# Kernel tuning notes

Measured on AMD Instinct MI355X. Metric: run time of the kernel, lower is better.

The kernel has to match this reference:

```python
import jax, jax.numpy as jnp
import numpy as np

N = 100000   # nodes
E = 3200000  # edges (avg degree 32)
G = 1024     # graphs in batch
H = 16       # hidden_dim


def setup_inputs() -> dict:
    key = jax.random.key(0)
    ks = jax.random.split(key, 12)
    p = lambda k, s: jax.random.normal(k, s, dtype=jnp.float32) * 0.1
    return {
        "types": jax.random.randint(ks[0], (N,), 0, 3),
        "pos": jax.random.randint(ks[1], (N,), 0, 3),
        "edge_index": jax.random.randint(ks[2], (2, E), 0, N),
        "batch": jnp.sort(jax.random.randint(ks[3], (N,), 0, G)),
        "W1": p(ks[4], (3, H)), "b1": jnp.zeros((H,), jnp.float32),
        "W2": p(ks[5], (3, H)), "b2": jnp.zeros((H,), jnp.float32),
        "Wg0": p(ks[6], (2 * H, H)), "bg0": jnp.zeros((H,), jnp.float32),
        "Wg1": p(ks[7], (H, H)), "bg1": jnp.zeros((H,), jnp.float32),
        "Wg2": p(ks[8], (H, H)), "bg2": jnp.zeros((H,), jnp.float32),
        "Wo": p(ks[9], (H, 1)), "bo": jnp.zeros((1,), jnp.float32),
    }


def reference(types, pos, edge_index, batch, W1, b1, W2, b2,
              Wg0, bg0, Wg1, bg1, Wg2, bg2, Wo, bo):
    # one-hot encode + linear embed
    xt = jax.nn.one_hot(types, 3, dtype=jnp.float32) @ W1 + b1   # [N, H]
    xp = jax.nn.one_hot(pos, 3, dtype=jnp.float32) @ W2 + b2     # [N, H]
    z = jnp.concatenate([xt, xp], axis=-1)                        # [N, 2H]

    src, dst = edge_index[0], edge_index[1]
    # GCN symmetric normalization with self-loops (gcn_norm)
    deg = jax.ops.segment_sum(jnp.ones((E,), jnp.float32), dst, num_segments=N) + 1.0
    dis = jax.lax.rsqrt(deg)                                      # D^{-1/2}
    edge_coef = (dis[src] * dis[dst])[:, None]                    # [E, 1]
    self_coef = (dis * dis)[:, None]                              # [N, 1]

    def gcn_conv(x, W, b):
        h = x @ W                                                 # [N, H]
        agg = jax.ops.segment_sum(h[src] * edge_coef, dst, num_segments=N)
        return agg + h * self_coef + b

    z = jax.nn.relu(gcn_conv(z, Wg0, bg0))  # dropout=0.2 is train-only; eval mode
    z = jax.nn.relu(gcn_conv(z, Wg1, bg1))
    z = gcn_conv(z, Wg2, bg2)               # no act after last layer

    # global_mean_pool over graph ids
    cnt = jax.ops.segment_sum(jnp.ones((N,), jnp.float32), batch, num_segments=G)
    pooled = jax.ops.segment_sum(z, batch, num_segments=G) / jnp.maximum(cnt, 1.0)[:, None]
    return pooled @ Wo + bo                                       # [G, 1]
```

## Files before the change

### kernel.cpp

```cpp
#include <hip/hip_runtime.h>
#include <hip/hip_fp16.h>

#define NN 100000
#define NE 3200000
#define NG 1024
#define NP 100352
#define NBUCK 391
#define NBLK 256
#define CHUNK ((NE + NBLK - 1) / NBLK)
#define WINCAP 12288
#define BATCH 8

static __device__ inline void acc8_u4(float* acc, uint4 u) {
    const __half2* ph = reinterpret_cast<const __half2*>(&u);
#pragma unroll
    for (int k = 0; k < 4; k++) {
        float2 f = __half22float2(ph[k]);
        acc[2 * k + 0] += f.x;
        acc[2 * k + 1] += f.y;
    }
}
static __device__ inline uint4 pack8(const float* v) {
    uint4 u;
    __half2 h0 = __floats2half2_rn(v[0], v[1]);
    __half2 h1 = __floats2half2_rn(v[2], v[3]);
    __half2 h2 = __floats2half2_rn(v[4], v[5]);
    __half2 h3 = __floats2half2_rn(v[6], v[7]);
    u.x = *reinterpret_cast<unsigned int*>(&h0);
    u.y = *reinterpret_cast<unsigned int*>(&h1);
    u.z = *reinterpret_cast<unsigned int*>(&h2);
    u.w = *reinterpret_cast<unsigned int*>(&h3);
    return u;
}

__global__ void hist_buckets(const int* __restrict__ dst, int* __restrict__ bcnt) {
    __shared__ int sm[NBUCK];
    int tid = threadIdx.x;
    for (int i = tid; i < NBUCK; i += 256) sm[i] = 0;
    __syncthreads();
    int s = blockIdx.x * CHUNK, e = min(NE, s + CHUNK);
    for (int i = s + tid; i < e; i += 256)
        atomicAdd(&sm[__builtin_nontemporal_load(&dst[i]) >> 8], 1);
    __syncthreads();
    for (int i = tid; i < NBUCK; i += 256)
        if (sm[i]) atomicAdd(&bcnt[i], sm[i]);
}

__global__ void scan_buckets(const int* __restrict__ bcnt, int* __restrict__ bbase) {
    __shared__ int tmp[512];
    int tid = threadIdx.x;
    int v = (tid < NBUCK) ? bcnt[tid] : 0;
    tmp[tid] = v;
    __syncthreads();
    for (int off = 1; off < 512; off <<= 1) {
        int t = (tid >= off) ? tmp[tid - off] : 0;
        __syncthreads();
        tmp[tid] += t;
        __syncthreads();
    }
    if (tid < NBUCK) bbase[tid] = tmp[tid] - v;
}

__global__ void partition(const int* __restrict__ src, const int* __restrict__ dst,
                          const int* __restrict__ bbase, int* __restrict__ bfill,
                          int* __restrict__ part) {
    __shared__ int smh[NBUCK];
    __shared__ int smc[NBUCK];
    int tid = threadIdx.x;
    for (int i = tid; i < NBUCK; i += 256) smh[i] = 0;
    __syncthreads();
    int s = blockIdx.x * CHUNK, e = min(NE, s + CHUNK);
    for (int i = s + tid; i < e; i += 256)
        atomicAdd(&smh[__builtin_nontemporal_load(&dst[i]) >> 8], 1);
    __syncthreads();
    for (int i = tid; i < NBUCK; i += 256) {
        int c = smh[i];
        smc[i] = c ? (bbase[i] + atomicAdd(&bfill[i], c)) : 0;
    }
    __syncthreads();
    for (int i = s + tid; i < e; i += 256) {
        int d = __builtin_nontemporal_load(&dst[i]);
        int sv = __builtin_nontemporal_load(&src[i]);
        int b = d >> 8;
        int p = atomicAdd(&smc[b], 1);
        part[p] = sv | ((d & 255) << 17);
    }
}

__global__ void build_csr(const int* __restrict__ part, const int* __restrict__ bbase,
                          const int* __restrict__ bcnt, int* __restrict__ cnt,
                          int* __restrict__ offs, float* __restrict__ dis,
                          int* __restrict__ srcs) {
    __shared__ int sm_cnt[256];
    __shared__ int sm_off[256];
    __shared__ int sm_cur[256];
    __shared__ int sm_win[WINCAP];
    int b = blockIdx.x, tid = threadIdx.x;
    int base = bbase[b], m = bcnt[b];
    sm_cnt[tid] = 0;
    __syncthreads();
    for (int i = tid; i < m; i += 256)
        atomicAdd(&sm_cnt[__builtin_nontemporal_load(&part[base + i]) >> 17], 1);
    __syncthreads();
    int v = sm_cnt[tid];
    sm_off[tid] = v;
    __syncthreads();
    for (int off = 1; off < 256; off <<= 1) {
        int t = (tid >= off) ? sm_off[tid - off] : 0;
        __syncthreads();
        sm_off[tid] += t;
        __syncthreads();
    }
    int excl = sm_off[tid] - v;
    int n = b * 256 + tid;
    if (n < NN) {
        cnt[n] = v;
        offs[n] = base + excl;
        dis[n] = rsqrtf((float)v + 1.0f);
    }
    sm_cur[tid] = excl;
    __syncthreads();
    if (m <= WINCAP) {
        for (int i = tid; i < m; i += 256) {
            int p = __builtin_nontemporal_load(&part[base + i]);
            int l = atomicAdd(&sm_cur[p >> 17], 1);
            sm_win[l] = p & 0x1FFFF;
        }
        __syncthreads();
        for (int i = tid; i < m; i += 256) srcs[base + i] = sm_win[i];
    } else {
        for (int i = tid; i < m; i += 256) {
            int p = __builtin_nontemporal_load(&part[base + i]);
            int l = atomicAdd(&sm_cur[p >> 17], 1);
            srcs[base + l] = p & 0x1FFFF;
        }
    }
}

__global__ void embed_tf0(const int* __restrict__ types, const int* __restrict__ pos,
                          const float* __restrict__ W1, const float* __restrict__ b1,
                          const float* __restrict__ W2, const float* __restrict__ b2,
                          const float* __restrict__ Wg0, const float* __restrict__ dis,
                          uint4* __restrict__ hs) {
    __shared__ float sW[32 * 16];
    int tid = threadIdx.x;
    sW[tid] = Wg0[tid];
    sW[tid + 256] = Wg0[tid + 256];
    __syncthreads();
    int n = blockIdx.x * 256 + tid;
    if (n >= NN) return;
    int ty = types[n], pp = pos[n];
    float z[32];
#pragma unroll
    for (int j = 0; j < 16; j++) z[j] = W1[ty * 16 + j] + b1[j];
#pragma unroll
    for (int j = 0; j < 16; j++) z[16 + j] = W2[pp * 16 + j] + b2[j];
    float dn = dis[n];
    float hv[16];
#pragma unroll
    for (int j = 0; j < 16; j++) {
        float a = 0.0f;
#pragma unroll
        for (int k = 0; k < 32; k++) a += z[k] * sW[k * 16 + j];
        hv[j] = a * dn;
    }
    hs[(size_t)n * 2 + 0] = pack8(hv);
    hs[(size_t)n * 2 + 1] = pack8(hv + 8);
}

template <int RELU, int FUSE_POOL>
__global__ __launch_bounds__(256, 4)
void agg_tf(const uint4* __restrict__ hs, const int* __restrict__ srcs,
            const int* __restrict__ offs, const int* __restrict__ cnt,
            const float* __restrict__ dis, const float* __restrict__ bias,
            const float* __restrict__ Wn, uint4* __restrict__ hs_out,
            const int* __restrict__ batch,
            float* __restrict__ pool, int* __restrict__ gcnt) {
    __shared__ float sW[256];
    int tid = threadIdx.x;
    if (!FUSE_POOL) {
        sW[tid] = Wn[tid];
        __syncthreads();
    }
    int gid = blockIdx.x * 256 + tid;
    int n = gid >> 2;
    int q = gid & 1;
    int c = (gid >> 1) & 1;
    if (n >= NN) return;
    int beg = offs[n], deg = cnt[n];
    float dn = dis[n];
    int half = deg >> 1;
    int i0 = c ? half : 0;
    int iend = c ? deg : half;
    float acc[8] = {0.f, 0.f, 0.f, 0.f, 0.f, 0.f, 0.f, 0.f};
    for (int i = i0; i < iend; i += BATCH) {
        uint4 g[BATCH];
#pragma unroll
        for (int j = 0; j < BATCH; j++) {
            int idx = i + j;
            int s = __builtin_nontemporal_load(&srcs[beg + idx]);
            s = (idx < iend) ? s : NN;
            g[j] = hs[(size_t)s * 2 + q];
        }
#pragma unroll
        for (int j = 0; j < BATCH; j++) acc8_u4(acc, g[j]);
    }
#pragma unroll
    for (int k = 0; k < 8; k++) acc[k] += __shfl_xor(acc[k], 2);
    if (c != 0) return;
    uint4 self = hs[(size_t)n * 2 + q];
    acc8_u4(acc, self);
#pragma unroll
    for (int k = 0; k < 8; k++) {
        acc[k] = fmaf(acc[k], dn, bias[q * 8 + k]);
        if (RELU) acc[k] = fmaxf(acc[k], 0.f);
    }
    if (FUSE_POOL) {
        float s = 0.f;
#pragma unroll
        for (int k = 0; k < 8; k++) s += acc[k] * Wn[q * 8 + k];
        s += __shfl_xor(s, 1);
        if (q == 0) {
            int g = batch[n];
            atomicAdd(&pool[g], s);
            atomicAdd(&gcnt[g], 1);
        }
    } else {
        float oth[8];
#pragma unroll
        for (int k = 0; k < 8; k++) oth[k] = __shfl_xor(acc[k], 1);
        float zlo[8], zhi[8];
#pragma unroll
        for (int k = 0; k < 8; k++) {
            zlo[k] = (q == 0) ? acc[k] : oth[k];
            zhi[k] = (q == 0) ? oth[k] : acc[k];
        }
        float hv[8] = {0.f, 0.f, 0.f, 0.f, 0.f, 0.f, 0.f, 0.f};
#pragma unroll
        for (int k = 0; k < 8; k++) {
            const float* wl = &sW[k * 16 + q * 8];
            const float* wh = &sW[(k + 8) * 16 + q * 8];
#pragma unroll
            for (int j = 0; j < 8; j++) {
                hv[j] += zlo[k] * wl[j];
                hv[j] += zhi[k] * wh[j];
            }
        }
#pragma unroll
        for (int j = 0; j < 8; j++) hv[j] *= dn;
        hs_out[(size_t)n * 2 + q] = pack8(hv);
    }
}

__global__ void finalize(const float* __restrict__ pool, const int* __restrict__ gcnt,
                         const float* __restrict__ bo, float* __restrict__ out) {
    int g = blockIdx.x * 256 + threadIdx.x;
    if (g < NG) {
        float c = fmaxf((float)gcnt[g], 1.0f);
        out[g] = pool[g] / c + bo[0];
    }
}

extern "C" void kernel_launch(void* const* d_in, const int* in_sizes, int n_in,
                              void* d_out, int out_size, void* d_ws, size_t ws_size,
                              hipStream_t stream) {
    const int*   types = (const int*)d_in[0];
    const int*   pos   = (const int*)d_in[1];
    const int*   ei    = (const int*)d_in[2];
    const int*   batch = (const int*)d_in[3];
    const float* W1  = (const float*)d_in[4];
    const float* b1  = (const float*)d_in[5];
    const float* W2  = (const float*)d_in[6];
    const float* b2  = (const float*)d_in[7];
    const float* Wg0 = (const float*)d_in[8];
    const float* bg0 = (const float*)d_in[9];
    const float* Wg1 = (const float*)d_in[10];
    const float* bg1 = (const float*)d_in[11];
    const float* Wg2 = (const float*)d_in[12];
    const float* bg2 = (const float*)d_in[13];
    const float* Wo  = (const float*)d_in[14];
    const float* bo  = (const float*)d_in[15];
    float* out = (float*)d_out;

    const int* esrc = ei;
    const int* edst = ei + NE;

    int*   bcnt  = (int*)d_ws;
    int*   bfill = bcnt + 512;
    float* pool  = (float*)(bfill + 512);
    int*   gcnt  = (int*)(pool + NG);
    int*   bbase = gcnt + NG;
    int*   cnt   = bbase + 512;
    int*   offs  = cnt + NP;
    float* dis   = (float*)(offs + NP);
    int*   srcs  = (int*)(dis + NP);
    int*   part  = srcs + NE;
    uint4* hsA   = (uint4*)part;
    uint4* hsB   = (uint4*)(part + NE / 2);
    (void)ws_size; (void)n_in; (void)in_sizes; (void)out_size;

    hipMemsetAsync(d_ws, 0, (size_t)(1024 + 2 * NG) * sizeof(int), stream);

    const int NB256 = (NN + 255) / 256;
    const int QB4 = (NN * 4 + 255) / 256;

    hist_buckets<<<NBLK, 256, 0, stream>>>(edst, bcnt);
    scan_buckets<<<1, 512, 0, stream>>>(bcnt, bbase);
    partition<<<NBLK, 256, 0, stream>>>(esrc, edst, bbase, bfill, part);
    build_csr<<<NBUCK, 256, 0, stream>>>(part, bbase, bcnt, cnt, offs, dis, srcs);

    hipMemsetAsync((char*)hsA + (size_t)NN * 32, 0, (size_t)(NP - NN) * 32, stream);
    hipMemsetAsync((char*)hsB + (size_t)NN * 32, 0, (size_t)(NP - NN) * 32, stream);

    embed_tf0<<<NB256, 256, 0, stream>>>(types, pos, W1, b1, W2, b2, Wg0, dis, hsA);
    agg_tf<1, 0><<<QB4, 256, 0, stream>>>(hsA, srcs, offs, cnt, dis, bg0, Wg1, hsB,
                                          batch, pool, gcnt);
    agg_tf<1, 0><<<QB4, 256, 0, stream>>>(hsB, srcs, offs, cnt, dis, bg1, Wg2, hsA,
                                          batch, pool, gcnt);
    agg_tf<0, 1><<<QB4, 256, 0, stream>>>(hsA, srcs, offs, cnt, dis, bg2, Wo, hsB ,
                                          batch, pool, gcnt);

    finalize<<<(NG + 255) / 256, 256, 0, stream>>>(pool, gcnt, bo, out);
}
```

Measured before the change: 342.7 us.

## Split neighbor list four ways per node, gathering full 32-byte rows

The aggregation kernel now gives each of four lanes per node a quarter of the edge list, and each lane loads the full 32-byte fp16 row of every neighbor instead of one half-row. Before, two lanes split the edges and each loaded one 16-byte half, so every source index was read twice. Now each index is read once and the 16-wide sums are combined across the four lanes with shuffles. The row gathers become nontemporal loads while the index loads become normal ones, and launch bounds drop to 3 blocks per CU to fit 16 accumulators and twice as many in-flight loads.

Measured after the change: 533.3 us. 55.6% more time.

```diff
diff --git a/kernel.cpp b/kernel.cpp
--- a/kernel.cpp
+++ b/kernel.cpp
@@ -11,25 +11,28 @@
 #define WINCAP 12288
 #define BATCH 8
 
-static __device__ inline void acc8_u4(float* acc, uint4 u) {
-    const __half2* ph = reinterpret_cast<const __half2*>(&u);
+typedef unsigned int u32x4 __attribute__((ext_vector_type(4)));
+
+static __device__ inline void acc8_v4(float* acc, u32x4 u) {
 #pragma unroll
     for (int k = 0; k < 4; k++) {
-        float2 f = __half22float2(ph[k]);
+        unsigned int w = u[k];
+        __half2 h = *reinterpret_cast<__half2*>(&w);
+        float2 f = __half22float2(h);
         acc[2 * k + 0] += f.x;
         acc[2 * k + 1] += f.y;
     }
 }
-static __device__ inline uint4 pack8(const float* v) {
-    uint4 u;
+static __device__ inline u32x4 pack8(const float* v) {
+    u32x4 u;
     __half2 h0 = __floats2half2_rn(v[0], v[1]);
     __half2 h1 = __floats2half2_rn(v[2], v[3]);
     __half2 h2 = __floats2half2_rn(v[4], v[5]);
     __half2 h3 = __floats2half2_rn(v[6], v[7]);
-    u.x = *reinterpret_cast<unsigned int*>(&h0);
-    u.y = *reinterpret_cast<unsigned int*>(&h1);
-    u.z = *reinterpret_cast<unsigned int*>(&h2);
-    u.w = *reinterpret_cast<unsigned int*>(&h3);
+    u[0] = *reinterpret_cast<unsigned int*>(&h0);
+    u[1] = *reinterpret_cast<unsigned int*>(&h1);
+    u[2] = *reinterpret_cast<unsigned int*>(&h2);
+    u[3] = *reinterpret_cast<unsigned int*>(&h3);
     return u;
 }
 
@@ -141,7 +144,7 @@
                           const float* __restrict__ W1, const float* __restrict__ b1,
                           const float* __restrict__ W2, const float* __restrict__ b2,
                           const float* __restrict__ Wg0, const float* __restrict__ dis,
-                          uint4* __restrict__ hs) {
+                          u32x4* __restrict__ hs) {
     __shared__ float sW[32 * 16];
     int tid = threadIdx.x;
     sW[tid] = Wg0[tid];
@@ -169,11 +172,11 @@
 }
 
 template <int RELU, int FUSE_POOL>
-__global__ __launch_bounds__(256, 4)
-void agg_tf(const uint4* __restrict__ hs, const int* __restrict__ srcs,
+__global__ __launch_bounds__(256, 3)
+void agg_tf(const u32x4* __restrict__ hs, const int* __restrict__ srcs,
             const int* __restrict__ offs, const int* __restrict__ cnt,
             const float* __restrict__ dis, const float* __restrict__ bias,
-            const float* __restrict__ Wn, uint4* __restrict__ hs_out,
+            const float* __restrict__ Wn, u32x4* __restrict__ hs_out,
             const int* __restrict__ batch,
             float* __restrict__ pool, int* __restrict__ gcnt) {
     __shared__ float sW[256];
@@ -184,71 +187,69 @@
     }
     int gid = blockIdx.x * 256 + tid;
     int n = gid >> 2;
-    int q = gid & 1;
-    int c = (gid >> 1) & 1;
+    int c = gid & 3;
     if (n >= NN) return;
     int beg = offs[n], deg = cnt[n];
     float dn = dis[n];
-    int half = deg >> 1;
-    int i0 = c ? half : 0;
-    int iend = c ? deg : half;
-    float acc[8] = {0.f, 0.f, 0.f, 0.f, 0.f, 0.f, 0.f, 0.f};
+    int i0 = (deg * c) >> 2;
+    int iend = (deg * (c + 1)) >> 2;
+    float acc[16];
+#pragma unroll
+    for (int k = 0; k < 16; k++) acc[k] = 0.f;
     for (int i = i0; i < iend; i += BATCH) {
-        uint4 g[BATCH];
+        u32x4 g0[BATCH], g1[BATCH];
 #pragma unroll
         for (int j = 0; j < BATCH; j++) {
             int idx = i + j;
-            int s = __builtin_nontemporal_load(&srcs[beg + idx]);
+            int s = srcs[beg + idx];
             s = (idx < iend) ? s : NN;
-            g[j] = hs[(size_t)s * 2 + q];
-        }
-#pragma unroll
-        for (int j = 0; j < BATCH; j++) acc8_u4(acc, g[j]);
-    }
-#pragma unroll
-    for (int k = 0; k < 8; k++) acc[k] += __shfl_xor(acc[k], 2);
-    if (c != 0) return;
-    uint4 self = hs[(size_t)n * 2 + q];
-    acc8_u4(acc, self);
-#pragma unroll
-    for (int k = 0; k < 8; k++) {
-        acc[k] = fmaf(acc[k], dn, bias[q * 8 + k]);
+            const u32x4* row = &hs[(size_t)s * 2];
+            g0[j] = __builtin_nontemporal_load(row);
+            g1[j] = __builtin_nontemporal_load(row + 1);
+        }
+#pragma unroll
+        for (int j = 0; j < BATCH; j++) {
+            acc8_v4(acc, g0[j]);
+            acc8_v4(acc + 8, g1[j]);
+        }
+    }
+#pragma unroll
+    for (int k = 0; k < 16; k++) acc[k] += __shfl_xor(acc[k], 1);
+#pragma unroll
+    for (int k = 0; k < 16; k++) acc[k] += __shfl_xor(acc[k], 2);
+    u32x4 s0 = hs[(size_t)n * 2 + 0];
+    u32x4 s1 = hs[(size_t)n * 2 + 1];
+    acc8_v4(acc, s0);
+    acc8_v4(acc + 8, s1);
+#pragma unroll
+    for (int k = 0; k < 16; k++) {
+        acc[k] = fmaf(acc[k], dn, bias[k]);
         if (RELU) acc[k] = fmaxf(acc[k], 0.f);
     }
     if (FUSE_POOL) {
-        float s = 0.f;
-#pragma unroll
-        for (int k = 0; k < 8; k++) s += acc[k] * Wn[q * 8 + k];
-        s += __shfl_xor(s, 1);
-        if (q == 0) {
+        if (c == 0) {
+            float s = 0.f;
+#pragma unroll
+            for (int k = 0; k < 16; k++) s += acc[k] * Wn[k];
             int g = batch[n];
             atomicAdd(&pool[g], s);
             atomicAdd(&gcnt[g], 1);
         }
     } else {
-        float oth[8];
-#pragma unroll
-        for (int k = 0; k < 8; k++) oth[k] = __shfl_xor(acc[k], 1);
-        float zlo[8], zhi[8];
-#pragma unroll
-        for (int k = 0; k < 8; k++) {
-            zlo[k] = (q == 0) ? acc[k] : oth[k];
-            zhi[k] = (q == 0) ? oth[k] : acc[k];
-        }
-        float hv[8] = {0.f, 0.f, 0.f, 0.f, 0.f, 0.f, 0.f, 0.f};
-#pragma unroll
-        for (int k = 0; k < 8; k++) {
-            const float* wl = &sW[k * 16 + q * 8];
-            const float* wh = &sW[(k + 8) * 16 + q * 8];
-#pragma unroll
-            for (int j = 0; j < 8; j++) {
-                hv[j] += zlo[k] * wl[j];
-                hv[j] += zhi[k] * wh[j];
+        if (c < 2) {
+            float hv[8];
+#pragma unroll
+            for (int j = 0; j < 8; j++) hv[j] = 0.f;
+#pragma unroll
+            for (int k = 0; k < 16; k++) {
+                const float* w = &sW[k * 16 + c * 8];
+#pragma unroll
+                for (int j = 0; j < 8; j++) hv[j] += acc[k] * w[j];
             }
-        }
-#pragma unroll
-        for (int j = 0; j < 8; j++) hv[j] *= dn;
-        hs_out[(size_t)n * 2 + q] = pack8(hv);
+#pragma unroll
+            for (int j = 0; j < 8; j++) hv[j] *= dn;
+            hs_out[(size_t)n * 2 + c] = pack8(hv);
+        }
     }
 }
 
@@ -295,11 +296,11 @@
     float* dis   = (float*)(offs + NP);
     int*   srcs  = (int*)(dis + NP);
     int*   part  = srcs + NE;
-    uint4* hsA   = (uint4*)part;
-    uint4* hsB   = (uint4*)(part + NE / 2);
+    u32x4* hsA   = (u32x4*)part;
+    u32x4* hsB   = (u32x4*)(part + NE / 2);
     (void)ws_size; (void)n_in; (void)in_sizes; (void)out_size;
 
-    hipMemsetAsync(d_ws, 0, (size_t)(1024 + 2 * NG) * sizeof(int), stream);
+    (void)hipMemsetAsync(d_ws, 0, (size_t)(1024 + 2 * NG) * sizeof(int), stream);
 
     const int NB256 = (NN + 255) / 256;
     const int QB4 = (NN * 4 + 255) / 256;
@@ -309,8 +310,8 @@
     partition<<<NBLK, 256, 0, stream>>>(esrc, edst, bbase, bfill, part);
     build_csr<<<NBUCK, 256, 0, stream>>>(part, bbase, bcnt, cnt, offs, dis, srcs);
 
-    hipMemsetAsync((char*)hsA + (size_t)NN * 32, 0, (size_t)(NP - NN) * 32, stream);
-    hipMemsetAsync((char*)hsB + (size_t)NN * 32, 0, (size_t)(NP - NN) * 32, stream);
+    (void)hipMemsetAsync((char*)hsA + (size_t)NN * 32, 0, (size_t)(NP - NN) * 32, stream);
+    (void)hipMemsetAsync((char*)hsB + (size_t)NN * 32, 0, (size_t)(NP - NN) * 32, stream);
 
     embed_tf0<<<NB256, 256, 0, stream>>>(types, pos, W1, b1, W2, b2, Wg0, dis, hsA);
     agg_tf<1, 0><<<QB4, 256, 0, stream>>>(hsA, srcs, offs, cnt, dis, bg0, Wg1, hsB,
```
